# Kernel tuning notes

Measured on AMD Instinct MI355X. Metric: run time of the kernel, lower is better.

Reference implementation:

```python
import jax, jax.numpy as jnp
import numpy as np
import math

HIDDEN = 1024
HEADS = 16
HEAD = HIDDEN // HEADS  # 64
SCALE_BASE = 512.0


def _gammas(heads):
    # 1 - exp(linspace(log(1/32), log(1/512), heads))
    return 1.0 - jnp.exp(jnp.linspace(math.log(1.0 / 32.0), math.log(1.0 / 512.0), heads))


def _xpos(x, downscale):
    # x: [B, H, S, d]  (same head_size d for every head -> shared tables)
    S, d = x.shape[2], x.shape[3]
    half = d // 2
    base_scale = (jnp.arange(0, d, 2, dtype=jnp.float32) + 0.4 * d) / (1.4 * d)  # [half]
    pos = jnp.arange(S, dtype=jnp.float32)
    scale = base_scale[None, :] ** (pos / SCALE_BASE)[:, None]  # [S, half]
    if downscale:
        scale = 1.0 / scale
    inv_freq = 1.0 / (10000.0 ** (jnp.arange(half, dtype=jnp.float32) / half))
    sinusoid = pos[:, None] * inv_freq[None, :]  # [S, half]
    # duplicate-interleave (each column repeated twice)
    sin = jnp.repeat(jnp.sin(sinusoid) * scale, 2, axis=-1)  # [S, d]
    cos = jnp.repeat(jnp.cos(sinusoid) * scale, 2, axis=-1)  # [S, d]
    x1 = x[..., ::2]
    x2 = x[..., 1::2]
    rot = jnp.stack([-x2, x1], axis=-1).reshape(x.shape)  # rotate_every_two
    return x * cos + rot * sin


def _decay_mask(S, gammas):
    # D[h, n, m] = gamma_h^(n-m) for n >= m else 0
    n = jnp.arange(S)[:, None]
    m = jnp.arange(S)[None, :]
    diff = (n - m).astype(jnp.float32)
    mask = (n >= m)
    pw = jnp.maximum(diff, 0.0)[None, :, :]  # avoid overflow on negative diffs
    return jnp.where(mask[None, :, :], gammas[:, None, None] ** pw, 0.0)  # [H, S, S]


def retention_forward(Q, K, V):
    B, S, _ = Q.shape
    # split heads: [B, S, HIDDEN] -> [B, H, S, HEAD]
    def split(x, hd):
        return x.reshape(B, S, HEADS, hd).transpose(0, 2, 1, 3)
    q = _xpos(split(Q, HEAD), downscale=False)
    k = _xpos(split(K, HEAD), downscale=True)
    v = split(V, HEAD)
    D = _decay_mask(S, _gammas(HEADS).astype(Q.dtype))  # [H, S, S]
    scores = jnp.einsum('bhsd,bhtd->bhst', q, k) * D[None]
    out = jnp.einsum('bhst,bhtd->bhsd', scores, v)
    return out.transpose(0, 2, 1, 3).reshape(B, S, HEADS * HEAD)


def setup_inputs() -> dict:
    key = jax.random.key(0)
    kq, kk, kv = jax.random.split(key, 3)
    B, S = 2, 2048
    return {
        'Q': jax.random.normal(kq, (B, S, HIDDEN), dtype=jnp.float32),
        'K': jax.random.normal(kk, (B, S, HIDDEN), dtype=jnp.float32),
        'V': jax.random.normal(kv, (B, S, HIDDEN), dtype=jnp.float32),
    }


def reference(Q, K, V):
    return retention_forward(Q, K, V)
```

## Files before the change

kernel.cpp:

```cpp
#include <hip/hip_runtime.h>
#include <hip/hip_bf16.h>
#include <math.h>

#define B_  2
#define S_  2048
#define H_  16
#define D_  64
#define SST 40

typedef __attribute__((ext_vector_type(8))) short bf16x8_t;
typedef __attribute__((ext_vector_type(4))) float f32x4_t;

__device__ __forceinline__ unsigned short f2bf(float f) {
    __hip_bfloat16 h = __float2bfloat16(f);
    return __builtin_bit_cast(unsigned short, h);
}

__device__ __forceinline__ void async16(const unsigned short* g, unsigned short* l) {
    __builtin_amdgcn_global_load_lds(
        (const __attribute__((address_space(1))) unsigned int*)g,
        (__attribute__((address_space(3))) unsigned int*)l, 16, 0, 0);
}

#define WAITV2 asm volatile("s_waitcnt vmcnt(2)" ::: "memory")
#define WAITV0 asm volatile("s_waitcnt vmcnt(0)" ::: "memory")
#define BAR    asm volatile("s_barrier" ::: "memory")

__global__ __launch_bounds__(256) void table_kernel(float4* __restrict__ rot4,
                                                    float2* __restrict__ g2) {
    int tid = blockIdx.x * 256 + threadIdx.x;
    int i   = tid & 31;
    int s   = tid >> 5;
    float pos = (float)s;

    float bsc  = (2.0f * (float)i + 25.6f) / 89.6f;
    float xsc  = exp2f(log2f(bsc) * pos * (1.0f / 512.0f));
    float invf = exp2f(-(float)i * (13.287712379549449f / 32.0f));
    float ang  = pos * invf;
    float kq = rintf(ang * 0.15915494309189535f);
    float r  = fmaf(kq, -6.2831853071795865f, ang);
    float sn = sinf(r), cs = cosf(r);
    float rxs = 1.0f / xsc;
    rot4[tid] = make_float4(cs * xsc, sn * xsc, cs * rxs, sn * rxs);

    if (tid < H_ * S_) {
        int hh = tid >> 11, ss = tid & 2047;
        float lnv   = -3.4657359027997265f + (float)hh * (-0.18483924814931874f);
        float l2g   = log2f(1.0f - expf(lnv));
        g2[tid] = make_float2(exp2f((float)ss * l2g), exp2f(-(float)ss * l2g));
    }
}

__global__ __launch_bounds__(256) void prep_kernel(const float* __restrict__ Q,
                                                   const float* __restrict__ K,
                                                   const float* __restrict__ V,
                                                   const float4* __restrict__ rot4,
                                                   const float2* __restrict__ g2,
                                                   unsigned short* __restrict__ qb,
                                                   unsigned short* __restrict__ kb,
                                                   unsigned short* __restrict__ vt) {
    __shared__ float tile[64 * 65];
    int t   = threadIdx.x;
    int bid = blockIdx.x;

    if (bid < 4096) {
        int r   = bid;
        int s   = r & 2047;
        int hh  = t >> 4;
        int i8  = t & 15;

        float4 r0 = rot4[s * 32 + 2 * i8];
        float4 r1 = rot4[s * 32 + 2 * i8 + 1];
        float2 g  = g2[hh * 2048 + s];

        long idx = (long)r * 1024 + t * 4;
        float4 xq = *(const float4*)(Q + idx);
        float4 xk = *(const float4*)(K + idx);

        float cq0 = r0.x * g.x, sq0 = r0.y * g.x;
        float ck0 = r0.z * g.y, sk0 = r0.w * g.y;
        float cq1 = r1.x * g.x, sq1 = r1.y * g.x;
        float ck1 = r1.z * g.y, sk1 = r1.w * g.y;

        float q0 = xq.x * cq0 - xq.y * sq0, q1 = xq.y * cq0 + xq.x * sq0;
        float q2 = xq.z * cq1 - xq.w * sq1, q3 = xq.w * cq1 + xq.z * sq1;
        float k0 = xk.x * ck0 - xk.y * sk0, k1 = xk.y * ck0 + xk.x * sk0;
        float k2 = xk.z * ck1 - xk.w * sk1, k3 = xk.w * ck1 + xk.z * sk1;

        *(uint2*)(qb + idx) = make_uint2((unsigned)f2bf(q0) | ((unsigned)f2bf(q1) << 16),
                                         (unsigned)f2bf(q2) | ((unsigned)f2bf(q3) << 16));
        *(uint2*)(kb + idx) = make_uint2((unsigned)f2bf(k0) | ((unsigned)f2bf(k1) << 16),
                                         (unsigned)f2bf(k2) | ((unsigned)f2bf(k3) << 16));
    } else {
        int vb = bid - 4096;
        int bh = vb & 31;
        int b = bh >> 4, hh = bh & 15;
        int s0 = (vb >> 5) * 64;

#pragma unroll
        for (int it = 0; it < 4; ++it) {
            int f  = it * 256 + t;
            int sl = f >> 4;
            int d4 = f & 15;
            float4 v = *(const float4*)(V + ((long)(b * S_ + s0 + sl)) * 1024 + hh * 64 + d4 * 4);
            tile[sl * 65 + d4 * 4 + 0] = v.x;
            tile[sl * 65 + d4 * 4 + 1] = v.y;
            tile[sl * 65 + d4 * 4 + 2] = v.z;
            tile[sl * 65 + d4 * 4 + 3] = v.w;
        }
        __syncthreads();
        int d = t >> 2, c = t & 3;
        unsigned int pk[8];
#pragma unroll
        for (int jj = 0; jj < 8; ++jj) {
            float f0 = tile[(c * 16 + 2 * jj + 0) * 65 + d];
            float f1 = tile[(c * 16 + 2 * jj + 1) * 65 + d];
            pk[jj] = (unsigned int)f2bf(f0) | ((unsigned int)f2bf(f1) << 16);
        }
        unsigned short* outp = vt + ((long)(bh * 64 + d)) * S_ + s0 + c * 16;
        ((uint4*)outp)[0] = make_uint4(pk[0], pk[1], pk[2], pk[3]);
        ((uint4*)outp)[1] = make_uint4(pk[4], pk[5], pk[6], pk[7]);
    }
}

__global__ __launch_bounds__(512, 4) void retention_kernel(const unsigned short* __restrict__ qb,
                                                           const unsigned short* __restrict__ kb,
                                                           const unsigned short* __restrict__ vt,
                                                           float* __restrict__ out) {
    __shared__ __align__(16) unsigned short KV[16384];
    __shared__ __align__(16) unsigned short Ss[8][32 * SST];
    unsigned short* K0 = KV;
    unsigned short* V0 = KV + 4096;
    unsigned short* K1 = KV + 8192;
    unsigned short* V1 = KV + 12288;

    int t = threadIdx.x;
    int w = t >> 6, lane = t & 63, quad = lane >> 4, l16 = lane & 15;
    int qw = w & 3;
    int p  = w >> 2;

    int i   = blockIdx.x;
    int bb0 = i & 1;
    int h4  = (i >> 1) & 15;
    int c3  = (i >> 5) & 7;
    int b8  = (i >> 8) & 1;
    int par = bb0 ^ b8;
    int g   = par ? (15 - h4) : h4;
    int bh  = c3 | (b8 << 3) | (bb0 << 4);
    int b = bh >> 4, hh = bh & 15;

    int q0w  = g * 128 + qw * 32;
    int dkt  = 2 * g + (qw >> 1);
    int odd  = qw & 1;
    int kvend = 2 * g + 2;

    const unsigned short* qB = qb + ((long)(b * S_ + q0w)) * 1024 + hh * 64;
    const unsigned short* kB = kb + ((long)(b * S_)) * 1024 + hh * 64;
    const unsigned short* vB = vt + (long)bh * 64 * S_;

    bf16x8_t aQ[2][2];
#pragma unroll
    for (int m = 0; m < 2; ++m)
#pragma unroll
        for (int kk = 0; kk < 2; ++kk)
            aQ[m][kk] = *(const bf16x8_t*)(qB + (long)(m * 16 + l16) * 1024 + kk * 32 + quad * 8);

    f32x4_t acc[2][4];
#pragma unroll
    for (int m = 0; m < 2; ++m)
#pragma unroll
        for (int nd = 0; nd < 4; ++nd) acc[m][nd] = (f32x4_t){0.f, 0.f, 0.f, 0.f};

    auto stage = [&](unsigned short* Kd, unsigned short* Vd, int kt) {
        const unsigned short* kSrc = kB + (long)kt * 64 * 1024;
        const unsigned short* vSrc = vB + kt * 64;
        int row = w * 8 + (lane >> 3);
        int c   = (lane & 7) ^ (row & 7);
        async16(kSrc + (long)row * 1024 + c * 8, Kd + w * 512);
        async16(vSrc + (long)row * S_ + c * 8, Vd + w * 512);
    };

    auto computeHalf = [&](const unsigned short* Kt, const unsigned short* Vt, bool diag) {
        f32x4_t sc[2][2];
#pragma unroll
        for (int m = 0; m < 2; ++m)
#pragma unroll
            for (int ntl = 0; ntl < 2; ++ntl) sc[m][ntl] = (f32x4_t){0.f, 0.f, 0.f, 0.f};

#pragma unroll
        for (int kk = 0; kk < 2; ++kk)
#pragma unroll
            for (int ntl = 0; ntl < 2; ++ntl) {
                int krow = p * 32 + ntl * 16 + l16;
                bf16x8_t bk = *(const bf16x8_t*)&Kt[krow * 64 +
                                                   (((kk * 4 + quad) ^ (krow & 7)) * 8)];
                sc[0][ntl] = __builtin_amdgcn_mfma_f32_16x16x32_bf16(aQ[0][kk], bk, sc[0][ntl], 0, 0, 0);
                sc[1][ntl] = __builtin_amdgcn_mfma_f32_16x16x32_bf16(aQ[1][kk], bk, sc[1][ntl], 0, 0, 0);
            }

        unsigned short* ssw = Ss[w];
        if (!diag) {
#pragma unroll
            for (int m = 0; m < 2; ++m)
#pragma unroll
                for (int ntl = 0; ntl < 2; ++ntl)
#pragma unroll
                    for (int r = 0; r < 4; ++r)
                        ssw[(m * 16 + quad * 4 + r) * SST + ntl * 16 + l16] = f2bf(sc[m][ntl][r]);
        } else {
#pragma unroll
            for (int m = 0; m < 2; ++m)
#pragma unroll
                for (int ntl = 0; ntl < 2; ++ntl) {
                    int dlt = (m - ntl) * 16;
#pragma unroll
                    for (int r = 0; r < 4; ++r) {
                        int rr = quad * 4 + r;
                        float v = ((rr + dlt) >= l16) ? sc[m][ntl][r] : 0.0f;
                        ssw[(m * 16 + rr) * SST + ntl * 16 + l16] = f2bf(v);
                    }
                }
        }

        bf16x8_t aS0 = *(const bf16x8_t*)&ssw[(0 * 16 + l16) * SST + quad * 8];
        bf16x8_t aS1 = *(const bf16x8_t*)&ssw[(1 * 16 + l16) * SST + quad * 8];
#pragma unroll
        for (int nd = 0; nd < 4; ++nd) {
            int vrow = nd * 16 + l16;
            bf16x8_t bv = *(const bf16x8_t*)&Vt[vrow * 64 +
                                               (((p * 4 + quad) ^ (vrow & 7)) * 8)];
            acc[0][nd] = __builtin_amdgcn_mfma_f32_16x16x32_bf16(aS0, bv, acc[0][nd], 0, 0, 0);
            acc[1][nd] = __builtin_amdgcn_mfma_f32_16x16x32_bf16(aS1, bv, acc[1][nd], 0, 0, 0);
        }
    };

    stage(K0, V0, 0);
    for (int kt = 0; kt < kvend; kt += 2) {
        stage(K1, V1, kt + 1);
        WAITV2;
        BAR;
        if (kt < dkt || (kt == dkt && p <= odd)) computeHalf(K0, V0, kt == dkt && p == odd);
        BAR;

        if (kt + 2 < kvend) { stage(K0, V0, kt + 2); WAITV2; }
        else                { WAITV0; }
        BAR;
        if (kt + 1 < dkt || (kt + 1 == dkt && p <= odd))
            computeHalf(K1, V1, kt + 1 == dkt && p == odd);
        BAR;
    }

    float* red = (float*)KV;
    if (p == 1) {
#pragma unroll
        for (int m = 0; m < 2; ++m)
#pragma unroll
            for (int nd = 0; nd < 4; ++nd)
#pragma unroll
                for (int r = 0; r < 4; ++r)
                    red[qw * 2048 + (m * 16 + quad * 4 + r) * 64 + nd * 16 + l16] = acc[m][nd][r];
    }
    BAR;
    if (p == 0) {
#pragma unroll
        for (int m = 0; m < 2; ++m)
#pragma unroll
            for (int nd = 0; nd < 4; ++nd)
#pragma unroll
                for (int r = 0; r < 4; ++r) {
                    int row = q0w + m * 16 + quad * 4 + r;
                    float v = acc[m][nd][r] +
                              red[qw * 2048 + (m * 16 + quad * 4 + r) * 64 + nd * 16 + l16];
                    out[((long)(b * S_ + row)) * 1024 + hh * 64 + nd * 16 + l16] = v;
                }
    }
}

extern "C" void kernel_launch(void* const* d_in, const int* in_sizes, int n_in,
                              void* d_out, int out_size, void* d_ws, size_t ws_size,
                              hipStream_t stream) {
    const float* Q = (const float*)d_in[0];
    const float* K = (const float*)d_in[1];
    const float* V = (const float*)d_in[2];
    float* out = (float*)d_out;

    const size_t perBuf = (size_t)B_ * H_ * S_ * D_;
    unsigned short* qb = (unsigned short*)d_ws;
    unsigned short* kb = qb + perBuf;
    unsigned short* vt = kb + perBuf;

    const size_t bufBytes = 3 * perBuf * sizeof(unsigned short);
    const size_t tblBytes = (size_t)S_ * 32 * sizeof(float4) + (size_t)H_ * S_ * sizeof(float2);
    char* tbl;
    if (ws_size >= bufBytes + tblBytes) tbl = (char*)d_ws + bufBytes;
    else                                tbl = (char*)d_out;
    float4* rot4 = (float4*)tbl;
    float2* g2   = (float2*)(rot4 + (size_t)S_ * 32);

    hipLaunchKernelGGL(table_kernel, dim3(256), dim3(256), 0, stream, rot4, g2);
    hipLaunchKernelGGL(prep_kernel, dim3(5120), dim3(256), 0, stream, Q, K, V, rot4, g2, qb, kb, vt);
    hipLaunchKernelGGL(retention_kernel, dim3(512), dim3(512), 0, stream, qb, kb, vt, out);
}
```

Before: 127.8 us.

## Fuse table generation into prep kernel and merge Q/K and V blocks

Removes the separate table kernel: each prep block now computes its own rotary and decay factors for 4 rows in shared memory. Each block also handles 4 Q/K rows plus one V-transpose tile, so the grid shrinks from 5120 to 1024 blocks. This drops one kernel launch and the global table round trip. In exchange every block recomputes transcendentals and adds an extra barrier.

```diff
diff --git a/kernel.cpp b/kernel.cpp
--- a/kernel.cpp
+++ b/kernel.cpp
@@ -26,76 +26,77 @@
 #define WAITV0 asm volatile("s_waitcnt vmcnt(0)" ::: "memory")
 #define BAR    asm volatile("s_barrier" ::: "memory")
 
-__global__ __launch_bounds__(256) void table_kernel(float4* __restrict__ rot4,
-                                                    float2* __restrict__ g2) {
-    int tid = blockIdx.x * 256 + threadIdx.x;
-    int i   = tid & 31;
-    int s   = tid >> 5;
-    float pos = (float)s;
-
-    float bsc  = (2.0f * (float)i + 25.6f) / 89.6f;
-    float xsc  = exp2f(log2f(bsc) * pos * (1.0f / 512.0f));
-    float invf = exp2f(-(float)i * (13.287712379549449f / 32.0f));
-    float ang  = pos * invf;
-    float kq = rintf(ang * 0.15915494309189535f);
-    float r  = fmaf(kq, -6.2831853071795865f, ang);
-    float sn = sinf(r), cs = cosf(r);
-    float rxs = 1.0f / xsc;
-    rot4[tid] = make_float4(cs * xsc, sn * xsc, cs * rxs, sn * rxs);
-
-    if (tid < H_ * S_) {
-        int hh = tid >> 11, ss = tid & 2047;
-        float lnv   = -3.4657359027997265f + (float)hh * (-0.18483924814931874f);
-        float l2g   = log2f(1.0f - expf(lnv));
-        g2[tid] = make_float2(exp2f((float)ss * l2g), exp2f(-(float)ss * l2g));
-    }
-}
-
 __global__ __launch_bounds__(256) void prep_kernel(const float* __restrict__ Q,
                                                    const float* __restrict__ K,
                                                    const float* __restrict__ V,
-                                                   const float4* __restrict__ rot4,
-                                                   const float2* __restrict__ g2,
                                                    unsigned short* __restrict__ qb,
                                                    unsigned short* __restrict__ kb,
                                                    unsigned short* __restrict__ vt) {
-    __shared__ float tile[64 * 65];
+    __shared__ float  tile[64 * 65];
+    __shared__ float4 rotq[4 * 32];
+    __shared__ float  gl[4 * 16 * 2];
     int t   = threadIdx.x;
     int bid = blockIdx.x;
 
-    if (bid < 4096) {
-        int r   = bid;
-        int s   = r & 2047;
-        int hh  = t >> 4;
-        int i8  = t & 15;
-
-        float4 r0 = rot4[s * 32 + 2 * i8];
-        float4 r1 = rot4[s * 32 + 2 * i8 + 1];
-        float2 g  = g2[hh * 2048 + s];
-
-        long idx = (long)r * 1024 + t * 4;
-        float4 xq = *(const float4*)(Q + idx);
-        float4 xk = *(const float4*)(K + idx);
-
-        float cq0 = r0.x * g.x, sq0 = r0.y * g.x;
-        float ck0 = r0.z * g.y, sk0 = r0.w * g.y;
-        float cq1 = r1.x * g.x, sq1 = r1.y * g.x;
-        float ck1 = r1.z * g.y, sk1 = r1.w * g.y;
-
-        float q0 = xq.x * cq0 - xq.y * sq0, q1 = xq.y * cq0 + xq.x * sq0;
-        float q2 = xq.z * cq1 - xq.w * sq1, q3 = xq.w * cq1 + xq.z * sq1;
-        float k0 = xk.x * ck0 - xk.y * sk0, k1 = xk.y * ck0 + xk.x * sk0;
-        float k2 = xk.z * ck1 - xk.w * sk1, k3 = xk.w * ck1 + xk.z * sk1;
-
-        *(uint2*)(qb + idx) = make_uint2((unsigned)f2bf(q0) | ((unsigned)f2bf(q1) << 16),
-                                         (unsigned)f2bf(q2) | ((unsigned)f2bf(q3) << 16));
-        *(uint2*)(kb + idx) = make_uint2((unsigned)f2bf(k0) | ((unsigned)f2bf(k1) << 16),
-                                         (unsigned)f2bf(k2) | ((unsigned)f2bf(k3) << 16));
+    if (t < 128) {
+        int sl = t >> 5, i = t & 31;
+        int s  = (bid * 4 + sl) & 2047;
+        float pos = (float)s;
+        float bsc  = (2.0f * (float)i + 25.6f) / 89.6f;
+        float xsc  = exp2f(log2f(bsc) * pos * (1.0f / 512.0f));
+        float invf = exp2f(-(float)i * (13.287712379549449f / 32.0f));
+        float ang  = pos * invf;
+        float kq = rintf(ang * 0.15915494309189535f);
+        float rr = fmaf(kq, -6.2831853071795865f, ang);
+        float sn = sinf(rr), cs = cosf(rr);
+        float rxs = 1.0f / xsc;
+        rotq[sl * 32 + i] = make_float4(cs * xsc, sn * xsc, cs * rxs, sn * rxs);
     } else {
-        int vb = bid - 4096;
-        int bh = vb & 31;
+        int u  = t - 128;
+        int sl = u >> 5, hh = (u >> 1) & 15, pm = u & 1;
+        int s  = (bid * 4 + sl) & 2047;
+        float lnv = -3.4657359027997265f + (float)hh * (-0.18483924814931874f);
+        float l2g = log2f(1.0f - expf(lnv));
+        gl[(sl * 16 + hh) * 2 + pm] = exp2f((pm ? -(float)s : (float)s) * l2g);
+    }
+    __syncthreads();
+
+    {
+        int hh = t >> 4, i8 = t & 15;
+#pragma unroll
+        for (int j = 0; j < 4; ++j) {
+            int r = bid * 4 + j;
+            float4 r0 = rotq[j * 32 + 2 * i8];
+            float4 r1 = rotq[j * 32 + 2 * i8 + 1];
+            float gx = gl[(j * 16 + hh) * 2 + 0];
+            float gy = gl[(j * 16 + hh) * 2 + 1];
+
+            long idx = (long)r * 1024 + t * 4;
+            float4 xq = *(const float4*)(Q + idx);
+            float4 xk = *(const float4*)(K + idx);
+
+            float cq0 = r0.x * gx, sq0 = r0.y * gx;
+            float ck0 = r0.z * gy, sk0 = r0.w * gy;
+            float cq1 = r1.x * gx, sq1 = r1.y * gx;
+            float ck1 = r1.z * gy, sk1 = r1.w * gy;
+
+            float q0 = xq.x * cq0 - xq.y * sq0, q1 = xq.y * cq0 + xq.x * sq0;
+            float q2 = xq.z * cq1 - xq.w * sq1, q3 = xq.w * cq1 + xq.z * sq1;
+            float k0 = xk.x * ck0 - xk.y * sk0, k1 = xk.y * ck0 + xk.x * sk0;
+            float k2 = xk.z * ck1 - xk.w * sk1, k3 = xk.w * ck1 + xk.z * sk1;
+
+            *(uint2*)(qb + idx) = make_uint2((unsigned)f2bf(q0) | ((unsigned)f2bf(q1) << 16),
+                                             (unsigned)f2bf(q2) | ((unsigned)f2bf(q3) << 16));
+            *(uint2*)(kb + idx) = make_uint2((unsigned)f2bf(k0) | ((unsigned)f2bf(k1) << 16),
+                                             (unsigned)f2bf(k2) | ((unsigned)f2bf(k3) << 16));
+        }
+    }
+    __syncthreads();
+
+    {
+        int bh = bid & 31;
         int b = bh >> 4, hh = bh & 15;
-        int s0 = (vb >> 5) * 64;
+        int s0 = (bid >> 5) * 64;
 
 #pragma unroll
         for (int it = 0; it < 4; ++it) {
@@ -289,15 +290,6 @@
     unsigned short* kb = qb + perBuf;
     unsigned short* vt = kb + perBuf;
 
-    const size_t bufBytes = 3 * perBuf * sizeof(unsigned short);
-    const size_t tblBytes = (size_t)S_ * 32 * sizeof(float4) + (size_t)H_ * S_ * sizeof(float2);
-    char* tbl;
-    if (ws_size >= bufBytes + tblBytes) tbl = (char*)d_ws + bufBytes;
-    else                                tbl = (char*)d_out;
-    float4* rot4 = (float4*)tbl;
-    float2* g2   = (float2*)(rot4 + (size_t)S_ * 32);
-
-    hipLaunchKernelGGL(table_kernel, dim3(256), dim3(256), 0, stream, rot4, g2);
-    hipLaunchKernelGGL(prep_kernel, dim3(5120), dim3(256), 0, stream, Q, K, V, rot4, g2, qb, kb, vt);
+    hipLaunchKernelGGL(prep_kernel, dim3(1024), dim3(256), 0, stream, Q, K, V, qb, kb, vt);
     hipLaunchKernelGGL(retention_kernel, dim3(512), dim3(512), 0, stream, qb, kb, vt, out);
 }
```

After: 125.4 us. About the same (-1.9%).
